# Kernel tuning notes

Measured on AMD Instinct MI355X. Metric: run time of the kernel, lower is better.

Reference implementation:

```python
import jax, jax.numpy as jnp
import numpy as np

VOCAB, EM_DIM, UNITS, BATCH, SEQ = 50000, 512, 1024, 64, 256


def setup_inputs() -> dict:
    key = jax.random.key(0)
    k_tok, k_emb, k_w, k_u, k_b = jax.random.split(key, 5)
    tokens = jax.random.randint(k_tok, (BATCH, SEQ), 0, VOCAB, dtype=jnp.int32)
    h0 = jnp.zeros((BATCH, UNITS), jnp.float32)
    c0 = jnp.zeros((BATCH, UNITS), jnp.float32)
    # learned params
    emb = jax.random.normal(k_emb, (VOCAB, EM_DIM), jnp.float32) * 0.05
    W = jax.random.normal(k_w, (EM_DIM, 4 * UNITS), jnp.float32) * 0.02   # input kernel, gate order [i,f,c,o]
    U = jax.random.normal(k_u, (UNITS, 4 * UNITS), jnp.float32) * 0.02    # recurrent kernel
    b = jnp.zeros((4 * UNITS,), jnp.float32)
    return {"tokens": tokens, "h0": h0, "c0": c0, "emb": emb, "W": W, "U": U, "b": b}


def _lstm_sigmoid(em, h0, c0, W, U, b):
    # em: [B, T, E] -> scan over time. Keras LSTM with activation='sigmoid':
    #   i,f,o = sigmoid(gates); g = sigmoid(candidate); c = f*c + i*g; h = o*sigmoid(c)
    n = h0.shape[-1]
    # precompute input projections for all timesteps (same math, one big GEMM)
    xz = jnp.einsum('bte,ef->btf', em, W) + b            # [B, T, 4U]
    xz = jnp.transpose(xz, (1, 0, 2))                     # [T, B, 4U]

    def step(carry, xz_t):
        h, c = carry
        z = xz_t + h @ U                                  # [B, 4U]
        i = jax.nn.sigmoid(z[:, :n])
        f = jax.nn.sigmoid(z[:, n:2 * n])
        g = jax.nn.sigmoid(z[:, 2 * n:3 * n])
        o = jax.nn.sigmoid(z[:, 3 * n:])
        c = f * c + i * g
        h = o * jax.nn.sigmoid(c)
        return (h, c), h

    (h, c), hs = jax.lax.scan(step, (h0, c0), xz)
    return jnp.transpose(hs, (1, 0, 2)), h, c             # output [B,T,U], h, c


def reference(tokens, h0, c0, emb, W, U, b):
    em = emb[tokens]                                      # embedding gather [B, T, E]
    output, h, c = _lstm_sigmoid(em, h0, c0, W, U, b)
    return output, h, c
```

## Files before the change

kernel.cpp:

```cpp
#include <hip/hip_runtime.h>
#include <stdint.h>


typedef __attribute__((ext_vector_type(8))) short short8;
typedef __attribute__((ext_vector_type(4))) float f32x4;
typedef __attribute__((ext_vector_type(4))) unsigned int u32x4;

#define NB 64
#define NT 256
#define NE 512
#define NU 1024
#define NG 4096
#define ROWS (NB*NT)

#define WS_EM    ((size_t)0)
#define WS_WT    ((size_t)16777216)
#define WS_UT    ((size_t)20971520)
#define WS_XZ    ((size_t)29360128)
#define WS_HBUF  ((size_t)163577856)
#define WS_FLAGS ((size_t)163840000)

#define SCAN_LDS_BYTES 131072

__device__ inline unsigned short f2bf(float x) {
    union { float f; uint32_t u; } v; v.f = x;
    uint32_t u = v.u;
    uint32_t r = u + 0x7FFFu + ((u >> 16) & 1u);
    return (unsigned short)(r >> 16);
}
__device__ inline unsigned int pack2bf(float a, float b) {
    return (unsigned int)f2bf(a) | ((unsigned int)f2bf(b) << 16);
}
__device__ inline float bf2f(unsigned short h) {
    union { uint32_t u; float f; } v; v.u = ((uint32_t)h) << 16;
    return v.f;
}
__device__ inline float sigmoidf(float z) { return 1.f / (1.f + __expf(-z)); }

__device__ inline void store_dword_sc(unsigned int* addr, unsigned int v) {
    asm volatile("global_store_dword %0, %1, off sc0 sc1" :: "v"(addr), "v"(v) : "memory");
}
__device__ inline u32x4 load_b128_sc(const unsigned int* addr) {
    u32x4 r;
    asm volatile("global_load_dwordx4 %0, %1, off sc0 sc1" : "=v"(r) : "v"(addr) : "memory");
    return r;
}
__device__ inline unsigned int load_dword_sc_wait(const unsigned int* addr) {
    unsigned int r;
    asm volatile("global_load_dword %0, %1, off sc0 sc1\n\ts_waitcnt vmcnt(0)"
                 : "=v"(r) : "v"(addr) : "memory");
    return r;
}
__device__ inline void wait_vm0() {
    asm volatile("s_waitcnt vmcnt(0)" ::: "memory");
}

__global__ void __launch_bounds__(256) transpose_cast_kernel(
    const float* __restrict__ in, unsigned int* __restrict__ out32,
    int K, int N) {
    __shared__ float tile[32][33];
    int k0 = blockIdx.x * 32, n0 = blockIdx.y * 32;
    int lx = threadIdx.x & 31, ly = threadIdx.x >> 5;
#pragma unroll
    for (int r = 0; r < 32; r += 8)
        tile[ly + r][lx] = in[(size_t)(k0 + ly + r) * N + n0 + lx];
    __syncthreads();
    int kp = threadIdx.x & 15, nl = threadIdx.x >> 4;
#pragma unroll
    for (int r = 0; r < 32; r += 16) {
        float lo = tile[2 * kp][nl + r], hi = tile[2 * kp + 1][nl + r];
        out32[((size_t)(n0 + nl + r) * K + k0) / 2 + kp] = pack2bf(lo, hi);
    }
}

__global__ void __launch_bounds__(256) gather_kernel(
    const int* __restrict__ tokens, const float* __restrict__ emb,
    unsigned int* __restrict__ em32) {
    int r = blockIdx.x;
    int tok = tokens[r];
    const float2* src = (const float2*)(emb + (size_t)tok * NE);
    unsigned int* dst = em32 + (size_t)r * (NE / 2);
    for (int i = threadIdx.x; i < NE / 2; i += 256) {
        float2 v = src[i];
        dst[i] = pack2bf(v.x, v.y);
    }
}

__global__ void __launch_bounds__(256) gemm1_kernel(
    const unsigned short* __restrict__ A, const unsigned short* __restrict__ BT,
    const float* __restrict__ bias, unsigned short* __restrict__ C) {
    __shared__ unsigned short As[128 * 64];
    __shared__ unsigned short Bs[128 * 64];
    int bid = blockIdx.x;
    int mb = bid & 127, nb = bid >> 7;
    int tid = threadIdx.x;
    int w = tid >> 6, l = tid & 63;
    int wm = w >> 1, wn = w & 1;

    f32x4 acc[4][4];
#pragma unroll
    for (int i = 0; i < 4; i++)
#pragma unroll
        for (int j = 0; j < 4; j++) acc[i][j] = f32x4{0.f, 0.f, 0.f, 0.f};

    for (int kt = 0; kt < 8; ++kt) {
        short8 av[4], bv[4];
#pragma unroll
        for (int r = 0; r < 4; ++r) {
            int chunk = r * 256 + tid;
            int row = chunk >> 3, c8 = chunk & 7;
            av[r] = *(const short8*)(A + ((size_t)(mb * 128 + row)) * NE + kt * 64 + c8 * 8);
            bv[r] = *(const short8*)(BT + ((size_t)(nb * 128 + row)) * NE + kt * 64 + c8 * 8);
        }
#pragma unroll
        for (int r = 0; r < 4; ++r) {
            int chunk = r * 256 + tid;
            *(short8*)(As + chunk * 8) = av[r];
            *(short8*)(Bs + chunk * 8) = bv[r];
        }
        __syncthreads();
#pragma unroll
        for (int kk = 0; kk < 2; ++kk) {
            short8 af[4], bf[4];
#pragma unroll
            for (int mi = 0; mi < 4; ++mi)
                af[mi] = *(const short8*)(As + (wm * 64 + mi * 16 + (l & 15)) * 64 + kk * 32 + (l >> 4) * 8);
#pragma unroll
            for (int ni = 0; ni < 4; ++ni)
                bf[ni] = *(const short8*)(Bs + (wn * 64 + ni * 16 + (l & 15)) * 64 + kk * 32 + (l >> 4) * 8);
#pragma unroll
            for (int mi = 0; mi < 4; ++mi)
#pragma unroll
                for (int ni = 0; ni < 4; ++ni)
                    acc[mi][ni] = __builtin_amdgcn_mfma_f32_16x16x32_bf16(af[mi], bf[ni], acc[mi][ni], 0, 0, 0);
        }
        __syncthreads();
    }
#pragma unroll
    for (int ni = 0; ni < 4; ++ni) {
        int col = nb * 128 + wn * 64 + ni * 16 + (l & 15);
        float bvv = bias[col];
#pragma unroll
        for (int mi = 0; mi < 4; ++mi) {
#pragma unroll
            for (int r = 0; r < 4; ++r) {
                int row = mb * 128 + wm * 64 + mi * 16 + ((l >> 4) * 4) + r;
                C[(size_t)row * NG + col] = f2bf(acc[mi][ni][r] + bvv);
            }
        }
    }
}

__global__ void __launch_bounds__(256, 1) scan_kernel(
    const unsigned short* __restrict__ UT,
    const unsigned short* __restrict__ XZ,
    const float* __restrict__ h0, const float* __restrict__ c0,
    unsigned int* hbuf32,
    unsigned int* flags,
    float* __restrict__ out) {
    extern __shared__ unsigned char smem[];
    unsigned short* Hs = (unsigned short*)smem;
    unsigned int* Hs32 = (unsigned int*)smem;
    float* zbuf = (float*)(smem + 32768);

    const int wg = blockIdx.x;
    const int p = wg >> 6, q = wg & 63;
    const int tid = threadIdx.x;
    const int g = tid >> 6;
    const int l = tid & 63;

    short8 Ufrag[32];
    {
        const unsigned short* urow =
            UT + ((size_t)(g * NU + q * 16 + (l & 15))) * NU + (l >> 4) * 8;
#pragma unroll
        for (int kt = 0; kt < 32; ++kt)
            Ufrag[kt] = *(const short8*)(urow + kt * 32);
    }

    const int bl = tid >> 4, ul = tid & 15;
    const int b = p * 16 + bl, u = q * 16 + ul;
    float c_reg = c0[(size_t)b * NU + u];
    {
        float hv = h0[(size_t)b * NU + u];
        unsigned short mybf = f2bf(hv);
        unsigned short obf = (unsigned short)__shfl_xor((int)mybf, 1, 64);
        if ((ul & 1) == 0) {
            int kt = u >> 5, grp = (u >> 3) & 3, j = u & 7;
            int fidx = (kt * 64 + grp * 16 + bl) * 8 + j;
            store_dword_sc(&hbuf32[(size_t)p * 8192 + (fidx >> 1)],
                           (unsigned int)mybf | ((unsigned int)obf << 16));
        }
    }
    wait_vm0();
    __syncthreads();
    if (tid == 0) store_dword_sc(&flags[wg], 1u);

    const unsigned short* xz_base = XZ + (size_t)(p * 16) * NT * NG + (size_t)(g * NU + q * 16);
    const int rb0 = (l >> 4) * 4, zc = l & 15;
    float* outO = out;
    float* outH = out + (size_t)NB * NT * NU;
    float* outC = outH + (size_t)NB * NU;

    for (int s = 0; s < NT; ++s) {
        float xv[4];
#pragma unroll
        for (int r = 0; r < 4; ++r)
            xv[r] = bf2f(xz_base[(size_t)((rb0 + r) * NT + s) * NG + zc]);

        if (tid < 64) {
            const unsigned int target = (unsigned int)(s + 1);
            const unsigned int* fl = &flags[p * 64 + tid];
            while (load_dword_sc_wait(fl) < target) {  }
        }
        __syncthreads();

        {
            const unsigned int* hb = hbuf32 + (size_t)((s & 1) * 4 + p) * 8192;
            u32x4 t[8];
#pragma unroll
            for (int k = 0; k < 8; ++k)
                t[k] = load_b128_sc(hb + k * 1024 + tid * 4);
            wait_vm0();
            __builtin_amdgcn_sched_barrier(0);
#pragma unroll
            for (int k = 0; k < 8; ++k)
                *(u32x4*)(Hs32 + k * 1024 + tid * 4) = t[k];
        }
        __syncthreads();

        f32x4 ac0 = f32x4{0.f, 0.f, 0.f, 0.f}, ac1 = ac0, ac2 = ac0, ac3 = ac0;
#pragma unroll
        for (int kt = 0; kt < 32; kt += 4) {
            short8 a0 = *(const short8*)(Hs + ((kt + 0) * 64 + l) * 8);
            short8 a1 = *(const short8*)(Hs + ((kt + 1) * 64 + l) * 8);
            short8 a2 = *(const short8*)(Hs + ((kt + 2) * 64 + l) * 8);
            short8 a3 = *(const short8*)(Hs + ((kt + 3) * 64 + l) * 8);
            ac0 = __builtin_amdgcn_mfma_f32_16x16x32_bf16(a0, Ufrag[kt + 0], ac0, 0, 0, 0);
            ac1 = __builtin_amdgcn_mfma_f32_16x16x32_bf16(a1, Ufrag[kt + 1], ac1, 0, 0, 0);
            ac2 = __builtin_amdgcn_mfma_f32_16x16x32_bf16(a2, Ufrag[kt + 2], ac2, 0, 0, 0);
            ac3 = __builtin_amdgcn_mfma_f32_16x16x32_bf16(a3, Ufrag[kt + 3], ac3, 0, 0, 0);
        }
        f32x4 acc = (ac0 + ac1) + (ac2 + ac3);

        {
#pragma unroll
            for (int r = 0; r < 4; ++r)
                zbuf[(g * 16 + rb0 + r) * 17 + zc] = acc[r] + xv[r];
        }
        __syncthreads();
        {
            float zi = zbuf[(0 * 16 + bl) * 17 + ul];
            float zf = zbuf[(1 * 16 + bl) * 17 + ul];
            float zg = zbuf[(2 * 16 + bl) * 17 + ul];
            float zo = zbuf[(3 * 16 + bl) * 17 + ul];
            float gi = sigmoidf(zi), gf = sigmoidf(zf);
            float gg = sigmoidf(zg), go = sigmoidf(zo);
            c_reg = gf * c_reg + gi * gg;
            float h = go * sigmoidf(c_reg);
            outO[((size_t)b * NT + s) * NU + u] = h;
            unsigned short mybf = f2bf(h);
            unsigned short obf = (unsigned short)__shfl_xor((int)mybf, 1, 64);
            if ((ul & 1) == 0) {
                int kt = u >> 5, grp = (u >> 3) & 3, j = u & 7;
                int fidx = (kt * 64 + grp * 16 + bl) * 8 + j;
                store_dword_sc(&hbuf32[(size_t)(((s + 1) & 1) * 4 + p) * 8192 + (fidx >> 1)],
                               (unsigned int)mybf | ((unsigned int)obf << 16));
            }
            if (s == NT - 1) {
                outH[(size_t)b * NU + u] = h;
                outC[(size_t)b * NU + u] = c_reg;
            }
        }
        wait_vm0();
        __syncthreads();
        if (tid == 0)
            store_dword_sc(&flags[wg], (unsigned int)(s + 2));
    }
}

extern "C" void kernel_launch(void* const* d_in, const int* in_sizes, int n_in,
                              void* d_out, int out_size, void* d_ws, size_t ws_size,
                              hipStream_t stream) {
    const int* tokens = (const int*)d_in[0];
    const float* h0 = (const float*)d_in[1];
    const float* c0 = (const float*)d_in[2];
    const float* emb = (const float*)d_in[3];
    const float* W = (const float*)d_in[4];
    const float* U = (const float*)d_in[5];
    const float* bias = (const float*)d_in[6];
    float* out = (float*)d_out;

    unsigned char* ws = (unsigned char*)d_ws;
    unsigned short* em_bf = (unsigned short*)(ws + WS_EM);
    unsigned short* WT = (unsigned short*)(ws + WS_WT);
    unsigned short* UT = (unsigned short*)(ws + WS_UT);
    unsigned short* XZ = (unsigned short*)(ws + WS_XZ);
    unsigned int* hbuf32 = (unsigned int*)(ws + WS_HBUF);
    unsigned int* flags = (unsigned int*)(ws + WS_FLAGS);

    hipMemsetAsync(flags, 0, 1024, stream);

    transpose_cast_kernel<<<dim3(NE / 32, NG / 32), 256, 0, stream>>>(W, (unsigned int*)WT, NE, NG);
    transpose_cast_kernel<<<dim3(NU / 32, NG / 32), 256, 0, stream>>>(U, (unsigned int*)UT, NU, NG);
    gather_kernel<<<ROWS, 256, 0, stream>>>(tokens, emb, (unsigned int*)em_bf);
    gemm1_kernel<<<4096, 256, 0, stream>>>(em_bf, WT, bias, XZ);

    hipFuncSetAttribute((const void*)scan_kernel,
                        hipFuncAttributeMaxDynamicSharedMemorySize, SCAN_LDS_BYTES);
    scan_kernel<<<256, 256, SCAN_LDS_BYTES, stream>>>(UT, XZ, h0, c0, hbuf32, flags, out);
}
```

Before: 1.358 ms.

## Replace flag-based step barrier with sentinel-filled per-step hidden-state ring

Adds a scan variant that writes each timestep's bf16 hidden state to its own slot in a 257-step ring, prefilled with a NaN sentinel. Consumers poll the data itself until no sentinel remains, which removes the flag polling, the extra syncthreads and the flag store from the recurrent critical path. The cost is a fill kernel over about 34 MB of ring memory before the scan, and the path depends on the workspace being large enough. A computed h whose bf16 pair exactly matches the sentinel would make a consumer spin forever.

```diff
diff --git a/kernel.cpp b/kernel.cpp
--- a/kernel.cpp
+++ b/kernel.cpp
@@ -19,6 +19,11 @@
 #define WS_XZ    ((size_t)29360128)
 #define WS_HBUF  ((size_t)163577856)
 #define WS_FLAGS ((size_t)163840000)
+#define WS_RING  ((size_t)163841024)
+#define RING_DWORDS ((size_t)257 * 4 * 8192)
+#define RING_BYTES  (RING_DWORDS * 4)
+
+#define SENT 0x7FC07FC0u
 
 #define SCAN_LDS_BYTES 131072
 
@@ -40,6 +45,9 @@
 __device__ inline void store_dword_sc(unsigned int* addr, unsigned int v) {
     asm volatile("global_store_dword %0, %1, off sc0 sc1" :: "v"(addr), "v"(v) : "memory");
 }
+__device__ inline void store_b128_sc(unsigned int* addr, u32x4 v) {
+    asm volatile("global_store_dwordx4 %0, %1, off sc0 sc1" :: "v"(addr), "v"(v) : "memory");
+}
 __device__ inline u32x4 load_b128_sc(const unsigned int* addr) {
     u32x4 r;
     asm volatile("global_load_dwordx4 %0, %1, off sc0 sc1" : "=v"(r) : "v"(addr) : "memory");
@@ -53,6 +61,13 @@
 }
 __device__ inline void wait_vm0() {
     asm volatile("s_waitcnt vmcnt(0)" ::: "memory");
+}
+
+__global__ void __launch_bounds__(256) fill_ring_kernel(unsigned int* p, size_t nvec4) {
+    u32x4 s4 = u32x4{SENT, SENT, SENT, SENT};
+    size_t stride = (size_t)gridDim.x * 256;
+    for (size_t i = blockIdx.x * 256 + threadIdx.x; i < nvec4; i += stride)
+        store_b128_sc(p + i * 4, s4);
 }
 
 __global__ void __launch_bounds__(256) transpose_cast_kernel(
@@ -151,13 +166,136 @@
     }
 }
 
+__global__ void __launch_bounds__(256, 1) scan_ring_kernel(
+    const unsigned short* __restrict__ UT,
+    const unsigned short* __restrict__ XZ,
+    const float* __restrict__ h0, const float* __restrict__ c0,
+    unsigned int* hring,
+    float* __restrict__ out) {
+    extern __shared__ unsigned char smem[];
+    unsigned short* Hs = (unsigned short*)smem;
+    unsigned int* Hs32 = (unsigned int*)smem;
+    float* zbuf = (float*)(smem + 32768);
+
+    const int wg = blockIdx.x;
+    const int p = wg >> 6, q = wg & 63;
+    const int tid = threadIdx.x;
+    const int g = tid >> 6;
+    const int l = tid & 63;
+
+    short8 Ufrag[32];
+    {
+        const unsigned short* urow =
+            UT + ((size_t)(g * NU + q * 16 + (l & 15))) * NU + (l >> 4) * 8;
+#pragma unroll
+        for (int kt = 0; kt < 32; ++kt)
+            Ufrag[kt] = *(const short8*)(urow + kt * 32);
+    }
+
+    const int bl = tid >> 4, ul = tid & 15;
+    const int b = p * 16 + bl, u = q * 16 + ul;
+    float c_reg = c0[(size_t)b * NU + u];
+    {
+        float hv = h0[(size_t)b * NU + u];
+        unsigned short mybf = f2bf(hv);
+        unsigned short obf = (unsigned short)__shfl_xor((int)mybf, 1, 64);
+        if ((ul & 1) == 0) {
+            int kt = u >> 5, grp = (u >> 3) & 3, j = u & 7;
+            int fidx = (kt * 64 + grp * 16 + bl) * 8 + j;
+            store_dword_sc(&hring[(size_t)p * 8192 + (fidx >> 1)],
+                           (unsigned int)mybf | ((unsigned int)obf << 16));
+        }
+    }
+
+    const unsigned short* xz_base = XZ + (size_t)(p * 16) * NT * NG + (size_t)(g * NU + q * 16);
+    const int rb0 = (l >> 4) * 4, zc = l & 15;
+    float* outO = out;
+    float* outH = out + (size_t)NB * NT * NU;
+    float* outC = outH + (size_t)NB * NU;
+
+    for (int s = 0; s < NT; ++s) {
+        float xv[4];
+#pragma unroll
+        for (int r = 0; r < 4; ++r)
+            xv[r] = bf2f(xz_base[(size_t)((rb0 + r) * NT + s) * NG + zc]);
+
+        const unsigned int* hb = hring + ((size_t)s * 4 + p) * 8192;
+        u32x4 t[8];
+#pragma unroll
+        for (int k = 0; k < 8; ++k)
+            t[k] = load_b128_sc(hb + k * 1024 + tid * 4);
+        wait_vm0();
+        for (;;) {
+            unsigned int badmask = 0;
+#pragma unroll
+            for (int k = 0; k < 8; ++k) {
+                u32x4 v = t[k];
+                if (v.x == SENT || v.y == SENT || v.z == SENT || v.w == SENT)
+                    badmask |= 1u << k;
+            }
+            if (!__any((int)(badmask != 0))) break;
+#pragma unroll
+            for (int k = 0; k < 8; ++k)
+                if (badmask & (1u << k))
+                    t[k] = load_b128_sc(hb + k * 1024 + tid * 4);
+            wait_vm0();
+        }
+        __builtin_amdgcn_sched_barrier(0);
+#pragma unroll
+        for (int k = 0; k < 8; ++k)
+            *(u32x4*)(Hs32 + k * 1024 + tid * 4) = t[k];
+        __syncthreads();
+
+        f32x4 ac0 = f32x4{0.f, 0.f, 0.f, 0.f}, ac1 = ac0, ac2 = ac0, ac3 = ac0;
+#pragma unroll
+        for (int kt = 0; kt < 32; kt += 4) {
+            short8 a0 = *(const short8*)(Hs + ((kt + 0) * 64 + l) * 8);
+            short8 a1 = *(const short8*)(Hs + ((kt + 1) * 64 + l) * 8);
+            short8 a2 = *(const short8*)(Hs + ((kt + 2) * 64 + l) * 8);
+            short8 a3 = *(const short8*)(Hs + ((kt + 3) * 64 + l) * 8);
+            ac0 = __builtin_amdgcn_mfma_f32_16x16x32_bf16(a0, Ufrag[kt + 0], ac0, 0, 0, 0);
+            ac1 = __builtin_amdgcn_mfma_f32_16x16x32_bf16(a1, Ufrag[kt + 1], ac1, 0, 0, 0);
+            ac2 = __builtin_amdgcn_mfma_f32_16x16x32_bf16(a2, Ufrag[kt + 2], ac2, 0, 0, 0);
+            ac3 = __builtin_amdgcn_mfma_f32_16x16x32_bf16(a3, Ufrag[kt + 3], ac3, 0, 0, 0);
+        }
+        f32x4 acc = (ac0 + ac1) + (ac2 + ac3);
+
+#pragma unroll
+        for (int r = 0; r < 4; ++r)
+            zbuf[(g * 16 + rb0 + r) * 17 + zc] = acc[r] + xv[r];
+        __syncthreads();
+
+        {
+            float zi = zbuf[(0 * 16 + bl) * 17 + ul];
+            float zf = zbuf[(1 * 16 + bl) * 17 + ul];
+            float zg = zbuf[(2 * 16 + bl) * 17 + ul];
+            float zo = zbuf[(3 * 16 + bl) * 17 + ul];
+            float gi = sigmoidf(zi), gf = sigmoidf(zf);
+            float gg = sigmoidf(zg), go = sigmoidf(zo);
+            c_reg = gf * c_reg + gi * gg;
+            float h = go * sigmoidf(c_reg);
+            unsigned short mybf = f2bf(h);
+            unsigned short obf = (unsigned short)__shfl_xor((int)mybf, 1, 64);
+            if ((ul & 1) == 0) {
+                int kt = u >> 5, grp = (u >> 3) & 3, j = u & 7;
+                int fidx = (kt * 64 + grp * 16 + bl) * 8 + j;
+                store_dword_sc(&hring[((size_t)(s + 1) * 4 + p) * 8192 + (fidx >> 1)],
+                               (unsigned int)mybf | ((unsigned int)obf << 16));
+            }
+            outO[((size_t)b * NT + s) * NU + u] = h;
+            if (s == NT - 1) {
+                outH[(size_t)b * NU + u] = h;
+                outC[(size_t)b * NU + u] = c_reg;
+            }
+        }
+    }
+}
+
 __global__ void __launch_bounds__(256, 1) scan_kernel(
     const unsigned short* __restrict__ UT,
     const unsigned short* __restrict__ XZ,
     const float* __restrict__ h0, const float* __restrict__ c0,
-    unsigned int* hbuf32,
-    unsigned int* flags,
-    float* __restrict__ out) {
+    unsigned int* hbuf32, unsigned int* flags, float* __restrict__ out) {
     extern __shared__ unsigned char smem[];
     unsigned short* Hs = (unsigned short*)smem;
     unsigned int* Hs32 = (unsigned int*)smem;
@@ -211,7 +349,7 @@
         if (tid < 64) {
             const unsigned int target = (unsigned int)(s + 1);
             const unsigned int* fl = &flags[p * 64 + tid];
-            while (load_dword_sc_wait(fl) < target) {  }
+            while (load_dword_sc_wait(fl) < target) { }
         }
         __syncthreads();
 
@@ -243,11 +381,9 @@
         }
         f32x4 acc = (ac0 + ac1) + (ac2 + ac3);
 
-        {
-#pragma unroll
-            for (int r = 0; r < 4; ++r)
-                zbuf[(g * 16 + rb0 + r) * 17 + zc] = acc[r] + xv[r];
-        }
+#pragma unroll
+        for (int r = 0; r < 4; ++r)
+            zbuf[(g * 16 + rb0 + r) * 17 + zc] = acc[r] + xv[r];
         __syncthreads();
         {
             float zi = zbuf[(0 * 16 + bl) * 17 + ul];
@@ -298,15 +434,24 @@
     unsigned short* XZ = (unsigned short*)(ws + WS_XZ);
     unsigned int* hbuf32 = (unsigned int*)(ws + WS_HBUF);
     unsigned int* flags = (unsigned int*)(ws + WS_FLAGS);
-
-    hipMemsetAsync(flags, 0, 1024, stream);
+    unsigned int* hring = (unsigned int*)(ws + WS_RING);
+
+    const bool use_ring = ws_size >= WS_RING + RING_BYTES;
 
     transpose_cast_kernel<<<dim3(NE / 32, NG / 32), 256, 0, stream>>>(W, (unsigned int*)WT, NE, NG);
     transpose_cast_kernel<<<dim3(NU / 32, NG / 32), 256, 0, stream>>>(U, (unsigned int*)UT, NU, NG);
     gather_kernel<<<ROWS, 256, 0, stream>>>(tokens, emb, (unsigned int*)em_bf);
     gemm1_kernel<<<4096, 256, 0, stream>>>(em_bf, WT, bias, XZ);
 
-    hipFuncSetAttribute((const void*)scan_kernel,
-                        hipFuncAttributeMaxDynamicSharedMemorySize, SCAN_LDS_BYTES);
-    scan_kernel<<<256, 256, SCAN_LDS_BYTES, stream>>>(UT, XZ, h0, c0, hbuf32, flags, out);
-}
+    if (use_ring) {
+        fill_ring_kernel<<<2048, 256, 0, stream>>>(hring, RING_DWORDS / 4);
+        hipFuncSetAttribute((const void*)scan_ring_kernel,
+                            hipFuncAttributeMaxDynamicSharedMemorySize, SCAN_LDS_BYTES);
+        scan_ring_kernel<<<256, 256, SCAN_LDS_BYTES, stream>>>(UT, XZ, h0, c0, hring, out);
+    } else {
+        hipMemsetAsync(flags, 0, 1024, stream);
+        hipFuncSetAttribute((const void*)scan_kernel,
+                            hipFuncAttributeMaxDynamicSharedMemorySize, SCAN_LDS_BYTES);
+        scan_kernel<<<256, 256, SCAN_LDS_BYTES, stream>>>(UT, XZ, h0, c0, hbuf32, flags, out);
+    }
+}
```

Measured after the change: 1.142 ms. -15.9%, faster.
